# Performance work log

Measured on AMD Instinct MI355X. Metric: run time of the kernel, lower is better.

## Reference

```python
import jax, jax.numpy as jnp
import numpy as np

T, S, B, H, NH, F = 256, 128, 32, 1024, 16, 4096
D = H // NH  # head dim


def setup_inputs() -> dict:
    key = jax.random.key(0)
    ks = jax.random.split(key, 14)
    w = lambda k, shape: jax.random.normal(k, shape, jnp.float32) * 0.02
    return {
        "x": jax.random.normal(ks[0], (T, B, H), jnp.float32),
        "src_bias": jnp.zeros((B, 1, 1, S), jnp.float32),
        "tgt_bias": jnp.zeros((B, 1, 1, T), jnp.float32),
        "memory": jax.random.normal(ks[1], (S, B, H), jnp.float32),
        # cross-attention projections
        "Wq": w(ks[2], (H, H)), "bq": jnp.zeros((H,), jnp.float32),
        "Wk": w(ks[3], (H, H)), "bk": jnp.zeros((H,), jnp.float32),
        "Wv": w(ks[4], (H, H)), "bv": jnp.zeros((H,), jnp.float32),
        "Wo": w(ks[5], (H, H)), "bo": jnp.zeros((H,), jnp.float32),
        # feed-forward
        "W1": w(ks[6], (H, F)), "b1": jnp.zeros((F,), jnp.float32),
        "W2": w(ks[7], (F, H)), "b2": jnp.zeros((H,), jnp.float32),
        # LSTM gates: input = cat(ffn_x, attn_ctx, h) -> 3H, output 4H (i,j,f,o)
        "Wg": w(ks[8], (3 * H, 4 * H)), "bg": jnp.zeros((4 * H,), jnp.float32),
    }


def _cross_attention(xq, mem, bias, Wq, bq, Wk, bk, Wv, bv, Wo, bo):
    # xq: [B,T,H], mem: [B,S,H], bias: [B,1,1,S]
    b, t, h = xq.shape
    q = (xq @ Wq + bq).reshape(b, t, NH, D) * (D ** -0.5)
    k = (mem @ Wk + bk).reshape(b, -1, NH, D)
    v = (mem @ Wv + bv).reshape(b, -1, NH, D)
    logits = jnp.einsum("bqhd,bkhd->bhqk", q, k) + bias
    wts = jax.nn.softmax(logits, axis=-1)
    ctx = jnp.einsum("bhqk,bkhd->bqhd", wts, v).reshape(b, t, h)
    return ctx @ Wo + bo


def reference(x, src_bias, tgt_bias, memory, Wq, bq, Wk, bk, Wv, bv, Wo, bo,
              W1, b1, W2, b2, Wg, bg):
    # cross attention (time-major -> batch-major -> time-major)
    c_attn = _cross_attention(jnp.transpose(x, (1, 0, 2)),
                              jnp.transpose(memory, (1, 0, 2)),
                              src_bias, Wq, bq, Wk, bk, Wv, bv, Wo, bo)
    c_attn = jnp.transpose(c_attn, (1, 0, 2))  # [T,B,H]

    # feed-forward on x (dropout disabled / eval mode)
    ffn_x = jax.nn.relu(x @ W1 + b1) @ W2 + b2  # [T,B,H]

    xs = jnp.concatenate([ffn_x, c_attn], axis=-1)  # [T,B,2H]
    c0 = jnp.zeros((x.shape[1], H), x.dtype)
    h0 = jnp.zeros((x.shape[1], H), x.dtype)

    def step(carry, xt):
        c, h = carry
        g = jnp.concatenate([xt, h], axis=-1) @ Wg + bg  # [B,4H]
        i = jax.nn.sigmoid(g[:, :H])
        j = jnp.tanh(g[:, H:2 * H])
        f = jax.nn.sigmoid(g[:, 2 * H:3 * H])
        o = jax.nn.sigmoid(g[:, 3 * H:])
        new_c = f * c + i * j
        new_h = o * new_c  # THUMT LSTMCell default activation=None
        return (new_c, new_h), new_h

    (c_f, h_f), hiddens = jax.lax.scan(step, (c0, h0), xs)
    return hiddens, c_f, h_f
```

## Files before the change

### kernel.cpp

```cpp
#include <hip/hip_runtime.h>
#include <cstdint>
#include <cstddef>

#define T_  256
#define S_  128
#define B_  32
#define H_  1024
#define NH_ 16
#define D_  64
#define F_  4096
#define TB_ (T_*B_)
#define SB_ (S_*B_)

typedef unsigned short u16;
typedef unsigned int   u32;
typedef unsigned long long u64;
typedef __attribute__((ext_vector_type(8))) short s16x8;
typedef __attribute__((ext_vector_type(4))) float f32x4;
typedef __attribute__((ext_vector_type(4))) u32  u32x4;

static __device__ __forceinline__ float b2f(u16 u) {
  union { u32 i; float f; } cv; cv.i = ((u32)u) << 16; return cv.f;
}
static __device__ __forceinline__ u16 f2b(float f) {
  union { float f; u32 i; } cv; cv.f = f;
  u32 u = cv.i;
  u32 r = (u + 0x7fffu + ((u >> 16) & 1u)) >> 16;
  return (u16)r;
}
static __device__ __forceinline__ float sigm(float x) {
  return 1.0f / (1.0f + __expf(-x));
}
static __device__ __forceinline__ float tanh_fast(float x) {
  float e2 = __expf(2.0f * x);
  return 1.0f - 2.0f / (e2 + 1.0f);
}

typedef const __attribute__((address_space(1))) void* gvoidp;
typedef __attribute__((address_space(3))) void* lvoidp;
static __device__ __forceinline__ void gl_lds16(const void* g, void* l) {
  __builtin_amdgcn_global_load_lds((gvoidp)g, (lvoidp)l, 16, 0, 0);
}

static __device__ __forceinline__ void cast_task(const float* __restrict__ in,
                                                 u16* __restrict__ out, int lb, int tid) {
  int i = lb * 256 + tid;
  float4 v = reinterpret_cast<const float4*>(in)[i];
  ushort4 o;
  o.x = f2b(v.x); o.y = f2b(v.y); o.z = f2b(v.z); o.w = f2b(v.w);
  reinterpret_cast<ushort4*>(out)[i] = o;
}

static __device__ __forceinline__ void tr32(const float* __restrict__ in,
                                            u16* __restrict__ out,
                                            int R, int C, int lin, int tid,
                                            float tile[32][33]) {
  const int gx = C >> 5;
  const int bx = lin % gx, by = lin / gx;
  const int c0 = bx << 5, r0 = by << 5;
  const int tx = tid & 31, ty = tid >> 5;
  #pragma unroll
  for (int k = 0; k < 32; k += 8)
    tile[ty + k][tx] = in[(size_t)(r0 + ty + k) * C + c0 + tx];
  __syncthreads();
  #pragma unroll
  for (int k = 0; k < 32; k += 8)
    out[(size_t)(c0 + ty + k) * R + r0 + tx] = f2b(tile[tx][ty + k]);
}

#define NB_SENT 1
#define NB_CX   8192
#define NB_CM   4096
#define NB_TSQ  1024
#define NB_TW1  4096
#define NB_TW2  4096
#define NB_TGX  8192
#define NB_TWH  4096
#define NB_PREP (NB_SENT + NB_CX + NB_CM + 4*NB_TSQ + NB_TW1 + NB_TW2 + NB_TGX + NB_TWH)

__global__ __launch_bounds__(256) void prep_all(
    const float* __restrict__ x, const float* __restrict__ mem,
    const float* __restrict__ Wq, const float* __restrict__ Wk,
    const float* __restrict__ Wv, const float* __restrict__ Wo,
    const float* __restrict__ W1, const float* __restrict__ W2,
    const float* __restrict__ Wg,
    u16* __restrict__ xb, u16* __restrict__ memb,
    u16* __restrict__ WqT, u16* __restrict__ WkT, u16* __restrict__ WvT,
    u16* __restrict__ WoT, u16* __restrict__ W1T, u16* __restrict__ W2T,
    u16* __restrict__ WgxT, u16* __restrict__ WhT, u32* __restrict__ sent)
{
  __shared__ float tile[32][33];
  int b = blockIdx.x;
  const int tid = threadIdx.x;
  if (b < NB_SENT) { sent[tid] = 0; sent[tid + 256] = 0; return; }
  b -= NB_SENT;
  if (b < NB_CX) { cast_task(x, xb, b, tid); return; }      b -= NB_CX;
  if (b < NB_CM) { cast_task(mem, memb, b, tid); return; }  b -= NB_CM;
  if (b < NB_TSQ) { tr32(Wq, WqT, H_, H_, b, tid, tile); return; }  b -= NB_TSQ;
  if (b < NB_TSQ) { tr32(Wk, WkT, H_, H_, b, tid, tile); return; }  b -= NB_TSQ;
  if (b < NB_TSQ) { tr32(Wv, WvT, H_, H_, b, tid, tile); return; }  b -= NB_TSQ;
  if (b < NB_TSQ) { tr32(Wo, WoT, H_, H_, b, tid, tile); return; }  b -= NB_TSQ;
  if (b < NB_TW1) { tr32(W1, W1T, H_, F_, b, tid, tile); return; }  b -= NB_TW1;
  if (b < NB_TW2) { tr32(W2, W2T, F_, H_, b, tid, tile); return; }  b -= NB_TW2;
  if (b < NB_TGX) { tr32(Wg, WgxT, 2 * H_, 4 * H_, b, tid, tile); return; } b -= NB_TGX;
  tr32(Wg + (size_t)(2 * H_) * (4 * H_), WhT, H_, 4 * H_, b, tid, tile);
}

#define SBAR      asm volatile("s_barrier" ::: "memory")
#define VMCNT4    asm volatile("s_waitcnt vmcnt(4)" ::: "memory")
#define VMCNT0    asm volatile("s_waitcnt vmcnt(0)" ::: "memory")

struct GJob {
  const u16* A; const u16* Bt; u16* Out; const float* bias;
  int Kdim; int ostride; int relu; int gridx; int nblk; float scale;
};
struct GBatch { GJob j[4]; int starts[4]; int njobs; };

static __device__ __forceinline__ void stage_region(
    const u16* __restrict__ src, int Kdim, int row0,
    int kt, int kh, char* lds_region, int tid) {
  const int w  = tid >> 6;
  const int r  = tid >> 2;
  const int cs = (tid & 3) ^ ((tid >> 3) & 3);
  const int kbase = kt * 64 + kh * 32 + cs * 8;
  gl_lds16(src + (size_t)(row0 + r) * Kdim + kbase,        lds_region + w * 1024);
  gl_lds16(src + (size_t)(row0 + 128 + r) * Kdim + kbase,  lds_region + 8192 + w * 1024);
}

static __device__ __forceinline__ s16x8 ldsf(const char* sm, int base, int row, int quad) {
  return *(const s16x8*)(sm + base + row * 64 + ((quad ^ ((row >> 1) & 3)) << 4));
}

__global__ __launch_bounds__(512, 2) void gemm256(GBatch gb)
{
  __shared__ __align__(16) u16 smem[65536];
  char* sm = (char*)smem;
  const int bid = blockIdx.x;
  int ji = 0;
  #pragma unroll
  for (int t = 1; t < 4; t++)
    if (t < gb.njobs && bid >= gb.starts[t]) ji = t;
  const GJob J = gb.j[ji];
  const int lin = bid - gb.starts[ji];
  const int wg = (lin & 7) * (J.nblk >> 3) + (lin >> 3);
  const int bx = wg % J.gridx, by = wg / J.gridx;
  const int bm = by << 8, bn = bx << 8;

  const int tid = threadIdx.x;
  const int wavei = tid >> 6, lane = tid & 63;
  const int quad = lane >> 4, l16 = lane & 15;
  const int wm = wavei >> 2, wn = wavei & 3;
  const int NT = J.Kdim >> 6;
  const int arow = wm * 128;
  const int brow = wn * 64;

  f32x4 acc[8][4] = {};

  stage_region(J.A,  J.Kdim, bm, 0, 0, sm + 0,     tid);
  stage_region(J.Bt, J.Kdim, bn, 0, 0, sm + 32768, tid);
  stage_region(J.A,  J.Kdim, bm, 0, 1, sm + 16384, tid);
  stage_region(J.Bt, J.Kdim, bn, 0, 1, sm + 49152, tid);
  VMCNT4;
  SBAR;

  for (int kt = 0; kt < NT; kt++) {
    const int p = (kt & 1) << 16;
    const int q = p ^ 65536;
    const int Ab = p, Bb = p + 32768;
    const bool st = (kt + 1 < NT);
    s16x8 af[8], b0, b1;

    #pragma unroll
    for (int mi = 0; mi < 8; mi++)
      af[mi] = ldsf(sm, Ab, arow + mi * 16 + l16, quad);
    b0 = ldsf(sm, Bb, brow + l16, quad);
    b1 = ldsf(sm, Bb, brow + 16 + l16, quad);
    if (st) stage_region(J.A, J.Kdim, bm, kt + 1, 0, sm + q, tid);
    SBAR;
    __builtin_amdgcn_s_setprio(1);
    #pragma unroll
    for (int mi = 0; mi < 8; mi++) {
      acc[mi][0] = __builtin_amdgcn_mfma_f32_16x16x32_bf16(af[mi], b0, acc[mi][0], 0, 0, 0);
      acc[mi][1] = __builtin_amdgcn_mfma_f32_16x16x32_bf16(af[mi], b1, acc[mi][1], 0, 0, 0);
    }
    __builtin_amdgcn_s_setprio(0);
    SBAR;

    b0 = ldsf(sm, Bb, brow + 32 + l16, quad);
    b1 = ldsf(sm, Bb, brow + 48 + l16, quad);
    if (st) stage_region(J.Bt, J.Kdim, bn, kt + 1, 0, sm + q + 32768, tid);
    SBAR;
    __builtin_amdgcn_s_setprio(1);
    #pragma unroll
    for (int mi = 0; mi < 8; mi++) {
      acc[mi][2] = __builtin_amdgcn_mfma_f32_16x16x32_bf16(af[mi], b0, acc[mi][2], 0, 0, 0);
      acc[mi][3] = __builtin_amdgcn_mfma_f32_16x16x32_bf16(af[mi], b1, acc[mi][3], 0, 0, 0);
    }
    __builtin_amdgcn_s_setprio(0);
    if (st) { VMCNT4; } else { VMCNT0; }
    SBAR;

    const int Ab1 = Ab + 16384, Bb1 = Bb + 16384;
    #pragma unroll
    for (int mi = 0; mi < 8; mi++)
      af[mi] = ldsf(sm, Ab1, arow + mi * 16 + l16, quad);
    b0 = ldsf(sm, Bb1, brow + l16, quad);
    b1 = ldsf(sm, Bb1, brow + 16 + l16, quad);
    if (st) stage_region(J.A, J.Kdim, bm, kt + 1, 1, sm + q + 16384, tid);
    SBAR;
    __builtin_amdgcn_s_setprio(1);
    #pragma unroll
    for (int mi = 0; mi < 8; mi++) {
      acc[mi][0] = __builtin_amdgcn_mfma_f32_16x16x32_bf16(af[mi], b0, acc[mi][0], 0, 0, 0);
      acc[mi][1] = __builtin_amdgcn_mfma_f32_16x16x32_bf16(af[mi], b1, acc[mi][1], 0, 0, 0);
    }
    __builtin_amdgcn_s_setprio(0);
    SBAR;

    b0 = ldsf(sm, Bb1, brow + 32 + l16, quad);
    b1 = ldsf(sm, Bb1, brow + 48 + l16, quad);
    if (st) stage_region(J.Bt, J.Kdim, bn, kt + 1, 1, sm + q + 49152, tid);
    SBAR;
    __builtin_amdgcn_s_setprio(1);
    #pragma unroll
    for (int mi = 0; mi < 8; mi++) {
      acc[mi][2] = __builtin_amdgcn_mfma_f32_16x16x32_bf16(af[mi], b0, acc[mi][2], 0, 0, 0);
      acc[mi][3] = __builtin_amdgcn_mfma_f32_16x16x32_bf16(af[mi], b1, acc[mi][3], 0, 0, 0);
    }
    __builtin_amdgcn_s_setprio(0);
    if (st) { VMCNT4; }
    SBAR;
  }

  #pragma unroll
  for (int mi = 0; mi < 8; mi++) {
    #pragma unroll
    for (int nj = 0; nj < 4; nj++) {
      const int colo = bn + wn * 64 + nj * 16 + l16;
      const float bv = J.bias[colo];
      #pragma unroll
      for (int r = 0; r < 4; r++) {
        const int rowo = bm + wm * 128 + mi * 16 + quad * 4 + r;
        float vv = (acc[mi][nj][r] + bv) * J.scale;
        if (J.relu) vv = fmaxf(vv, 0.0f);
        J.Out[(size_t)rowo * J.ostride + colo] = f2b(vv);
      }
    }
  }
}

__global__ __launch_bounds__(256) void attn_kernel(
    const u16* __restrict__ q, const u16* __restrict__ k, const u16* __restrict__ v,
    const float* __restrict__ src_bias, u16* __restrict__ ctx)
{
  __shared__ u16 ks[S_ * D_];
  __shared__ u16 vs[S_ * D_];
  const int b  = blockIdx.x >> 4;
  const int nh = blockIdx.x & 15;
  const int tid = threadIdx.x;

  for (int i = tid; i < (S_ * D_) / 8; i += 256) {
    int s = i >> 3, c = (i & 7) * 8;
    *(uint4*)&ks[s * D_ + c] = *(const uint4*)&k[((size_t)(s * B_ + b)) * H_ + nh * D_ + c];
    *(uint4*)&vs[s * D_ + c] = *(const uint4*)&v[((size_t)(s * B_ + b)) * H_ + nh * D_ + c];
  }
  __syncthreads();

  const int t = tid;
  float qf[D_];
  const u16* qp = &q[((size_t)(t * B_ + b)) * H_ + nh * D_];
  #pragma unroll
  for (int c8 = 0; c8 < D_; c8 += 8) {
    uint4 qv = *(const uint4*)&qp[c8];
    const u16* pu = (const u16*)&qv;
    #pragma unroll
    for (int j = 0; j < 8; j++) qf[c8 + j] = b2f(pu[j]);
  }
  const float* bias = src_bias + b * S_;

  float m = -1e30f, l = 0.0f;
  for (int s = 0; s < S_; s++) {
    float dot = 0.0f;
    #pragma unroll
    for (int d = 0; d < D_; d++) dot += qf[d] * b2f(ks[s * D_ + d]);
    dot += bias[s];
    float nm = fmaxf(m, dot);
    l = l * __expf(m - nm) + __expf(dot - nm);
    m = nm;
  }
  float of[D_] = {};
  const float inv = 1.0f / l;
  for (int s = 0; s < S_; s++) {
    float dot = 0.0f;
    #pragma unroll
    for (int d = 0; d < D_; d++) dot += qf[d] * b2f(ks[s * D_ + d]);
    dot += bias[s];
    float w = __expf(dot - m) * inv;
    #pragma unroll
    for (int d = 0; d < D_; d++) of[d] += w * b2f(vs[s * D_ + d]);
  }
  u16* op = &ctx[((size_t)(t * B_ + b)) * H_ + nh * D_];
  #pragma unroll
  for (int c8 = 0; c8 < D_; c8 += 8) {
    u16 tmp[8];
    #pragma unroll
    for (int j = 0; j < 8; j++) tmp[j] = f2b(of[c8 + j]);
    *(uint4*)&op[c8] = *(const uint4*)tmp;
  }
}

#define ISSUE2(K) { \
  const u16* b0_ = hb + ((size_t)(wave * 16 + (K) * 2 + (quad >> 1))) * 512 + \
                   (quad & 1) * 8 + l16 * 16; \
  asm volatile("global_load_dwordx4 %0, %1, off sc0 sc1" : "=v"(ba[K][0]) : "v"(b0_) : "memory"); \
  asm volatile("global_load_dwordx4 %0, %1, off sc0 sc1" : "=v"(ba[K][1]) : "v"(b0_ + 256) : "memory"); }

#define DO_MFMA(A0,A1,KC)                                                           \
  { _Pragma("unroll") for (int g_ = 0; g_ < 3; g_++) {                              \
      s16x8 wf_ = *(const s16x8*)&Wl[wave][((g_ * 8 + (KC)) * 64 + lane) * 8];      \
      acc[g_][0] = __builtin_amdgcn_mfma_f32_16x16x32_bf16(A0, wf_, acc[g_][0], 0, 0, 0); \
      acc[g_][1] = __builtin_amdgcn_mfma_f32_16x16x32_bf16(A1, wf_, acc[g_][1], 0, 0, 0); } \
    acc[3][0] = __builtin_amdgcn_mfma_f32_16x16x32_bf16(A0, wo[KC], acc[3][0], 0, 0, 0);  \
    acc[3][1] = __builtin_amdgcn_mfma_f32_16x16x32_bf16(A1, wo[KC], acc[3][1], 0, 0, 0); }

#define CONSUME(K, NSTR) { \
  asm volatile("s_waitcnt vmcnt(" NSTR ")" ::: "memory"); \
  __builtin_amdgcn_sched_barrier(0); \
  DO_MFMA(ba[K][0], ba[K][1], K); }

__global__ __launch_bounds__(256, 1) void lstm_persistent(
    const u16* __restrict__ g_x, const u16* __restrict__ WhT,
    u16* __restrict__ hb16, u32* __restrict__ sent, float* __restrict__ out)
{
  __shared__ __align__(16) u16 Wl[4][3 * 8 * 64 * 8];
  __shared__ float P[4][4][32][17];
  const int bk = blockIdx.x, tid = threadIdx.x;
  const int wave = tid >> 6, lane = tid & 63;
  const int quad = lane >> 4, l16 = lane & 15;

  for (int i = lane; i < 3 * 8 * 64; i += 64) {
    const int g  = (i >> 9) & 3;
    const int kc = (i >> 6) & 7;
    const int row = g * H_ + bk * 16 + (lane & 15);
    const int col = wave * 256 + kc * 32 + (lane >> 4) * 8;
    *(uint4*)&Wl[wave][i * 8] = *(const uint4*)&WhT[(size_t)row * H_ + col];
  }
  s16x8 wo[8];
  {
    const int row = 3 * H_ + bk * 16 + (lane & 15);
    const int colb = wave * 256 + (lane >> 4) * 8;
    #pragma unroll
    for (int kc = 0; kc < 8; kc++)
      wo[kc] = *(const s16x8*)&WhT[(size_t)row * H_ + colb + kc * 32];
  }
  __syncthreads();

  const int pb = tid >> 4, pc = tid & 15;
  const int col = bk * 16 + pc;
  float creg[2] = {0.0f, 0.0f};

  float gxp[2][4];
  #pragma unroll
  for (int ii = 0; ii < 2; ii++)
    #pragma unroll
    for (int g = 0; g < 4; g++)
      gxp[ii][g] = b2f(g_x[((size_t)(pb + ii * 16)) * (4 * H_) + g * H_ + col]);

  s16x8 ba[8][2];

  for (int t = 0; t < T_; t++) {
    if (t > 0) {
      const u32 st = (u32)t;
      const u16* hb = hb16 + ((t & 1) ^ 1) * 32768;

      { const u32* sp = sent + ((size_t)(((t & 1) ^ 1) * 256 + wave * 64 + lane));
        u32 sv;
        do {
          asm volatile("global_load_dword %0, %1, off sc0 sc1\n\ts_waitcnt vmcnt(0)"
                       : "=v"(sv) : "v"(sp) : "memory");
        } while (!__all(sv == st)); }

      f32x4 acc[4][2] = {};
      ISSUE2(0) ISSUE2(1) ISSUE2(2) ISSUE2(3)
      ISSUE2(4) ISSUE2(5) ISSUE2(6) ISSUE2(7)
      CONSUME(0, "14") CONSUME(1, "12") CONSUME(2, "10") CONSUME(3, "8")
      CONSUME(4, "6")  CONSUME(5, "4")  CONSUME(6, "2")  CONSUME(7, "0")

      #pragma unroll
      for (int g = 0; g < 4; g++)
        #pragma unroll
        for (int mt = 0; mt < 2; mt++)
          #pragma unroll
          for (int r = 0; r < 4; r++)
            P[wave][g][mt * 16 + quad * 4 + r][l16] = acc[g][mt][r];
    }
    __syncthreads();

    float gs[2][4];
    #pragma unroll
    for (int ii = 0; ii < 2; ii++) {
      const int b_ = pb + ii * 16;
      #pragma unroll
      for (int g = 0; g < 4; g++) {
        float s = gxp[ii][g];
        if (t > 0) s += P[0][g][b_][pc] + P[1][g][b_][pc] + P[2][g][b_][pc] + P[3][g][b_][pc];
        gs[ii][g] = s;
      }
    }
    __syncthreads();

    float hn[2], cn[2];
    #pragma unroll
    for (int ii = 0; ii < 2; ii++) {
      const float iv = sigm(gs[ii][0]);
      const float jv = tanh_fast(gs[ii][1]);
      const float fv = sigm(gs[ii][2]);
      const float ov = sigm(gs[ii][3]);
      cn[ii] = fv * creg[ii] + iv * jv;
      hn[ii] = ov * cn[ii];
      creg[ii] = cn[ii];
    }

    {
      u32 lo0 = f2b(hn[0]), lo1 = f2b(hn[1]);
      u32 hi0 = __shfl_down(lo0, 1), hi1 = __shfl_down(lo1, 1);
      if ((pc & 1) == 0) {
        u32* hw32 = (u32*)(hb16 + (t & 1) * 32768);
        u32 dw0 = lo0 | (hi0 << 16);
        u32 dw1 = lo1 | (hi1 << 16);
        __hip_atomic_store(&hw32[(size_t)bk * 256 + pb * 8 + (pc >> 1)], dw0,
                           __ATOMIC_RELAXED, __HIP_MEMORY_SCOPE_AGENT);
        __hip_atomic_store(&hw32[(size_t)bk * 256 + (pb + 16) * 8 + (pc >> 1)], dw1,
                           __ATOMIC_RELAXED, __HIP_MEMORY_SCOPE_AGENT);
      }
      asm volatile("s_waitcnt vmcnt(0)" ::: "memory");
      if (lane == 0)
        __hip_atomic_store(&sent[(size_t)(t & 1) * 256 + bk * 4 + wave], (u32)(t + 1),
                           __ATOMIC_RELAXED, __HIP_MEMORY_SCOPE_AGENT);
    }

    #pragma unroll
    for (int ii = 0; ii < 2; ii++) {
      const int b_ = pb + ii * 16;
      out[(size_t)t * (B_ * H_) + b_ * H_ + col] = hn[ii];
      if (t == T_ - 1) {
        out[(size_t)T_ * B_ * H_ + b_ * H_ + col] = cn[ii];
        out[(size_t)T_ * B_ * H_ + B_ * H_ + b_ * H_ + col] = hn[ii];
      }
    }
    if (t < T_ - 1) {
      #pragma unroll
      for (int ii = 0; ii < 2; ii++)
        #pragma unroll
        for (int g = 0; g < 4; g++)
          gxp[ii][g] = b2f(g_x[((size_t)(t + 1) * B_ + pb + ii * 16) * (4 * H_) + g * H_ + col]);
    }
  }
}

extern "C" void kernel_launch(void* const* d_in, const int* in_sizes, int n_in,
                              void* d_out, int out_size, void* d_ws, size_t ws_size,
                              hipStream_t stream)
{
  const float* x        = (const float*)d_in[0];
  const float* src_bias = (const float*)d_in[1];
  const float* mem      = (const float*)d_in[3];
  const float* Wq = (const float*)d_in[4];  const float* bq = (const float*)d_in[5];
  const float* Wk = (const float*)d_in[6];  const float* bk = (const float*)d_in[7];
  const float* Wv = (const float*)d_in[8];  const float* bv = (const float*)d_in[9];
  const float* Wo = (const float*)d_in[10]; const float* bo = (const float*)d_in[11];
  const float* W1 = (const float*)d_in[12]; const float* b1f = (const float*)d_in[13];
  const float* W2 = (const float*)d_in[14]; const float* b2f_ = (const float*)d_in[15];
  const float* Wg = (const float*)d_in[16]; const float* bg = (const float*)d_in[17];
  float* out = (float*)d_out;

  char* p = (char*)d_ws;
  u16* xb   = (u16*)p; p += (size_t)TB_ * H_ * 2;
  u16* memb = (u16*)p; p += (size_t)SB_ * H_ * 2;
  u16* WqT  = (u16*)p; p += (size_t)H_ * H_ * 2;
  u16* WkT  = (u16*)p; p += (size_t)H_ * H_ * 2;
  u16* WvT  = (u16*)p; p += (size_t)H_ * H_ * 2;
  u16* WoT  = (u16*)p; p += (size_t)H_ * H_ * 2;
  u16* W1T  = (u16*)p; p += (size_t)F_ * H_ * 2;
  u16* W2T  = (u16*)p; p += (size_t)H_ * F_ * 2;
  u16* WgxT = (u16*)p; p += (size_t)(4 * H_) * (2 * H_) * 2;
  u16* WhT  = (u16*)p; p += (size_t)(4 * H_) * H_ * 2;
  u16* qb   = (u16*)p; p += (size_t)TB_ * H_ * 2;
  u16* kb   = (u16*)p; p += (size_t)SB_ * H_ * 2;
  u16* vb   = (u16*)p; p += (size_t)SB_ * H_ * 2;
  u16* ctxb = (u16*)p; p += (size_t)TB_ * H_ * 2;
  u16* xs   = (u16*)p; p += (size_t)TB_ * (2 * H_) * 2;
  u16* h1   = (u16*)p; p += (size_t)TB_ * F_ * 2;
  u16* hb16 = (u16*)p; p += (size_t)2 * 32768 * 2;
  u32* sent = (u32*)p; p += (size_t)2 * 256 * 4;
  u16* gx   = h1;

  prep_all<<<dim3(NB_PREP), dim3(256), 0, stream>>>(
      x, mem, Wq, Wk, Wv, Wo, W1, W2, Wg,
      xb, memb, WqT, WkT, WvT, WoT, W1T, W2T, WgxT, WhT, sent);

  GBatch gb1 = {};
  gb1.j[0] = { xb,   WqT, qb, bq,  H_, H_, 0, H_ / 256, (TB_ / 256) * (H_ / 256), 0.125f };
  gb1.j[1] = { memb, WkT, kb, bk,  H_, H_, 0, H_ / 256, (SB_ / 256) * (H_ / 256), 1.0f   };
  gb1.j[2] = { memb, WvT, vb, bv,  H_, H_, 0, H_ / 256, (SB_ / 256) * (H_ / 256), 1.0f   };
  gb1.j[3] = { xb,   W1T, h1, b1f, H_, F_, 1, F_ / 256, (TB_ / 256) * (F_ / 256), 1.0f   };
  gb1.starts[0] = 0;
  gb1.starts[1] = gb1.j[0].nblk;
  gb1.starts[2] = gb1.starts[1] + gb1.j[1].nblk;
  gb1.starts[3] = gb1.starts[2] + gb1.j[2].nblk;
  gb1.njobs = 4;
  const int nb1 = gb1.starts[3] + gb1.j[3].nblk;
  gemm256<<<dim3(nb1), dim3(512), 0, stream>>>(gb1);

  attn_kernel<<<dim3(B_ * NH_), dim3(256), 0, stream>>>(qb, kb, vb, src_bias, ctxb);

  GBatch gb2 = {};
  gb2.j[0] = { ctxb, WoT, xs + H_, bo,   H_, 2 * H_, 0, H_ / 256, (TB_ / 256) * (H_ / 256), 1.0f };
  gb2.j[1] = { h1,   W2T, xs,      b2f_, F_, 2 * H_, 0, H_ / 256, (TB_ / 256) * (H_ / 256), 1.0f };
  gb2.starts[0] = 0;
  gb2.starts[1] = gb2.j[0].nblk;
  gb2.njobs = 2;
  const int nb2 = gb2.starts[1] + gb2.j[1].nblk;
  gemm256<<<dim3(nb2), dim3(512), 0, stream>>>(gb2);

  GBatch gb3 = {};
  gb3.j[0] = { xs, WgxT, gx, bg, 2 * H_, 4 * H_, 0, 4 * H_ / 256, (TB_ / 256) * (4 * H_ / 256), 1.0f };
  gb3.starts[0] = 0;
  gb3.njobs = 1;
  gemm256<<<dim3(gb3.j[0].nblk), dim3(512), 0, stream>>>(gb3);

  lstm_persistent<<<dim3(64), dim3(256), 0, stream>>>(gx, WhT, hb16, sent, out);
}
```

Measured before the change: 1.591 ms.

## Fuse gate-input GEMM into persistent LSTM kernel with per-tile readiness flags

Merges the final gate-input GEMM and the persistent LSTM recurrence into one launch. 64 blocks run the recurrence while the other 512 blocks compute the gx tiles in row order and publish per-tile ready flags. The recurrence polls a flag every 8 timesteps before loading gx, so it can start before the whole GEMM is done and the two overlap. In exchange the LSTM blocks now use 512 threads with half idle, LDS grows, and correctness depends on the LSTM blocks being co-resident with the GEMM blocks.

```diff
diff --git a/kernel.cpp b/kernel.cpp
--- a/kernel.cpp
+++ b/kernel.cpp
@@ -87,12 +87,17 @@
     u16* __restrict__ xb, u16* __restrict__ memb,
     u16* __restrict__ WqT, u16* __restrict__ WkT, u16* __restrict__ WvT,
     u16* __restrict__ WoT, u16* __restrict__ W1T, u16* __restrict__ W2T,
-    u16* __restrict__ WgxT, u16* __restrict__ WhT, u32* __restrict__ sent)
+    u16* __restrict__ WgxT, u16* __restrict__ WhT, u32* __restrict__ sent,
+    u32* __restrict__ gxs)
 {
   __shared__ float tile[32][33];
   int b = blockIdx.x;
   const int tid = threadIdx.x;
-  if (b < NB_SENT) { sent[tid] = 0; sent[tid + 256] = 0; return; }
+  if (b < NB_SENT) {
+    sent[tid] = 0; sent[tid + 256] = 0;
+    gxs[tid] = 0;  gxs[tid + 256] = 0;
+    return;
+  }
   b -= NB_SENT;
   if (b < NB_CX) { cast_task(x, xb, b, tid); return; }      b -= NB_CX;
   if (b < NB_CM) { cast_task(mem, memb, b, tid); return; }  b -= NB_CM;
@@ -129,6 +134,93 @@
 
 static __device__ __forceinline__ s16x8 ldsf(const char* sm, int base, int row, int quad) {
   return *(const s16x8*)(sm + base + row * 64 + ((quad ^ ((row >> 1) & 3)) << 4));
+}
+
+static __device__ __forceinline__ void gemm_compute(
+    const GJob& J, int bm, int bn, char* sm, f32x4 (&acc)[8][4], int tid)
+{
+  const int wavei = tid >> 6, lane = tid & 63;
+  const int quad = lane >> 4, l16 = lane & 15;
+  const int wm = wavei >> 2, wn = wavei & 3;
+  const int NT = J.Kdim >> 6;
+  const int arow = wm * 128;
+  const int brow = wn * 64;
+
+  stage_region(J.A,  J.Kdim, bm, 0, 0, sm + 0,     tid);
+  stage_region(J.Bt, J.Kdim, bn, 0, 0, sm + 32768, tid);
+  stage_region(J.A,  J.Kdim, bm, 0, 1, sm + 16384, tid);
+  stage_region(J.Bt, J.Kdim, bn, 0, 1, sm + 49152, tid);
+  VMCNT4;
+  SBAR;
+
+  for (int kt = 0; kt < NT; kt++) {
+    const int p = (kt & 1) << 16;
+    const int q = p ^ 65536;
+    const int Ab = p, Bb = p + 32768;
+    const bool st = (kt + 1 < NT);
+    s16x8 af[8], b0, b1;
+
+    #pragma unroll
+    for (int mi = 0; mi < 8; mi++)
+      af[mi] = ldsf(sm, Ab, arow + mi * 16 + l16, quad);
+    b0 = ldsf(sm, Bb, brow + l16, quad);
+    b1 = ldsf(sm, Bb, brow + 16 + l16, quad);
+    if (st) stage_region(J.A, J.Kdim, bm, kt + 1, 0, sm + q, tid);
+    SBAR;
+    __builtin_amdgcn_s_setprio(1);
+    #pragma unroll
+    for (int mi = 0; mi < 8; mi++) {
+      acc[mi][0] = __builtin_amdgcn_mfma_f32_16x16x32_bf16(af[mi], b0, acc[mi][0], 0, 0, 0);
+      acc[mi][1] = __builtin_amdgcn_mfma_f32_16x16x32_bf16(af[mi], b1, acc[mi][1], 0, 0, 0);
+    }
+    __builtin_amdgcn_s_setprio(0);
+    SBAR;
+
+    b0 = ldsf(sm, Bb, brow + 32 + l16, quad);
+    b1 = ldsf(sm, Bb, brow + 48 + l16, quad);
+    if (st) stage_region(J.Bt, J.Kdim, bn, kt + 1, 0, sm + q + 32768, tid);
+    SBAR;
+    __builtin_amdgcn_s_setprio(1);
+    #pragma unroll
+    for (int mi = 0; mi < 8; mi++) {
+      acc[mi][2] = __builtin_amdgcn_mfma_f32_16x16x32_bf16(af[mi], b0, acc[mi][2], 0, 0, 0);
+      acc[mi][3] = __builtin_amdgcn_mfma_f32_16x16x32_bf16(af[mi], b1, acc[mi][3], 0, 0, 0);
+    }
+    __builtin_amdgcn_s_setprio(0);
+    if (st) { VMCNT4; } else { VMCNT0; }
+    SBAR;
+
+    const int Ab1 = Ab + 16384, Bb1 = Bb + 16384;
+    #pragma unroll
+    for (int mi = 0; mi < 8; mi++)
+      af[mi] = ldsf(sm, Ab1, arow + mi * 16 + l16, quad);
+    b0 = ldsf(sm, Bb1, brow + l16, quad);
+    b1 = ldsf(sm, Bb1, brow + 16 + l16, quad);
+    if (st) stage_region(J.A, J.Kdim, bm, kt + 1, 1, sm + q + 16384, tid);
+    SBAR;
+    __builtin_amdgcn_s_setprio(1);
+    #pragma unroll
+    for (int mi = 0; mi < 8; mi++) {
+      acc[mi][0] = __builtin_amdgcn_mfma_f32_16x16x32_bf16(af[mi], b0, acc[mi][0], 0, 0, 0);
+      acc[mi][1] = __builtin_amdgcn_mfma_f32_16x16x32_bf16(af[mi], b1, acc[mi][1], 0, 0, 0);
+    }
+    __builtin_amdgcn_s_setprio(0);
+    SBAR;
+
+    b0 = ldsf(sm, Bb1, brow + 32 + l16, quad);
+    b1 = ldsf(sm, Bb1, brow + 48 + l16, quad);
+    if (st) stage_region(J.Bt, J.Kdim, bn, kt + 1, 1, sm + q + 49152, tid);
+    SBAR;
+    __builtin_amdgcn_s_setprio(1);
+    #pragma unroll
+    for (int mi = 0; mi < 8; mi++) {
+      acc[mi][2] = __builtin_amdgcn_mfma_f32_16x16x32_bf16(af[mi], b0, acc[mi][2], 0, 0, 0);
+      acc[mi][3] = __builtin_amdgcn_mfma_f32_16x16x32_bf16(af[mi], b1, acc[mi][3], 0, 0, 0);
+    }
+    __builtin_amdgcn_s_setprio(0);
+    if (st) { VMCNT4; }
+    SBAR;
+  }
 }
 
 __global__ __launch_bounds__(512, 2) void gemm256(GBatch gb)
@@ -145,92 +237,13 @@
   const int wg = (lin & 7) * (J.nblk >> 3) + (lin >> 3);
   const int bx = wg % J.gridx, by = wg / J.gridx;
   const int bm = by << 8, bn = bx << 8;
-
   const int tid = threadIdx.x;
   const int wavei = tid >> 6, lane = tid & 63;
   const int quad = lane >> 4, l16 = lane & 15;
   const int wm = wavei >> 2, wn = wavei & 3;
-  const int NT = J.Kdim >> 6;
-  const int arow = wm * 128;
-  const int brow = wn * 64;
 
   f32x4 acc[8][4] = {};
-
-  stage_region(J.A,  J.Kdim, bm, 0, 0, sm + 0,     tid);
-  stage_region(J.Bt, J.Kdim, bn, 0, 0, sm + 32768, tid);
-  stage_region(J.A,  J.Kdim, bm, 0, 1, sm + 16384, tid);
-  stage_region(J.Bt, J.Kdim, bn, 0, 1, sm + 49152, tid);
-  VMCNT4;
-  SBAR;
-
-  for (int kt = 0; kt < NT; kt++) {
-    const int p = (kt & 1) << 16;
-    const int q = p ^ 65536;
-    const int Ab = p, Bb = p + 32768;
-    const bool st = (kt + 1 < NT);
-    s16x8 af[8], b0, b1;
-
-    #pragma unroll
-    for (int mi = 0; mi < 8; mi++)
-      af[mi] = ldsf(sm, Ab, arow + mi * 16 + l16, quad);
-    b0 = ldsf(sm, Bb, brow + l16, quad);
-    b1 = ldsf(sm, Bb, brow + 16 + l16, quad);
-    if (st) stage_region(J.A, J.Kdim, bm, kt + 1, 0, sm + q, tid);
-    SBAR;
-    __builtin_amdgcn_s_setprio(1);
-    #pragma unroll
-    for (int mi = 0; mi < 8; mi++) {
-      acc[mi][0] = __builtin_amdgcn_mfma_f32_16x16x32_bf16(af[mi], b0, acc[mi][0], 0, 0, 0);
-      acc[mi][1] = __builtin_amdgcn_mfma_f32_16x16x32_bf16(af[mi], b1, acc[mi][1], 0, 0, 0);
-    }
-    __builtin_amdgcn_s_setprio(0);
-    SBAR;
-
-    b0 = ldsf(sm, Bb, brow + 32 + l16, quad);
-    b1 = ldsf(sm, Bb, brow + 48 + l16, quad);
-    if (st) stage_region(J.Bt, J.Kdim, bn, kt + 1, 0, sm + q + 32768, tid);
-    SBAR;
-    __builtin_amdgcn_s_setprio(1);
-    #pragma unroll
-    for (int mi = 0; mi < 8; mi++) {
-      acc[mi][2] = __builtin_amdgcn_mfma_f32_16x16x32_bf16(af[mi], b0, acc[mi][2], 0, 0, 0);
-      acc[mi][3] = __builtin_amdgcn_mfma_f32_16x16x32_bf16(af[mi], b1, acc[mi][3], 0, 0, 0);
-    }
-    __builtin_amdgcn_s_setprio(0);
-    if (st) { VMCNT4; } else { VMCNT0; }
-    SBAR;
-
-    const int Ab1 = Ab + 16384, Bb1 = Bb + 16384;
-    #pragma unroll
-    for (int mi = 0; mi < 8; mi++)
-      af[mi] = ldsf(sm, Ab1, arow + mi * 16 + l16, quad);
-    b0 = ldsf(sm, Bb1, brow + l16, quad);
-    b1 = ldsf(sm, Bb1, brow + 16 + l16, quad);
-    if (st) stage_region(J.A, J.Kdim, bm, kt + 1, 1, sm + q + 16384, tid);
-    SBAR;
-    __builtin_amdgcn_s_setprio(1);
-    #pragma unroll
-    for (int mi = 0; mi < 8; mi++) {
-      acc[mi][0] = __builtin_amdgcn_mfma_f32_16x16x32_bf16(af[mi], b0, acc[mi][0], 0, 0, 0);
-      acc[mi][1] = __builtin_amdgcn_mfma_f32_16x16x32_bf16(af[mi], b1, acc[mi][1], 0, 0, 0);
-    }
-    __builtin_amdgcn_s_setprio(0);
-    SBAR;
-
-    b0 = ldsf(sm, Bb1, brow + 32 + l16, quad);
-    b1 = ldsf(sm, Bb1, brow + 48 + l16, quad);
-    if (st) stage_region(J.Bt, J.Kdim, bn, kt + 1, 1, sm + q + 49152, tid);
-    SBAR;
-    __builtin_amdgcn_s_setprio(1);
-    #pragma unroll
-    for (int mi = 0; mi < 8; mi++) {
-      acc[mi][2] = __builtin_amdgcn_mfma_f32_16x16x32_bf16(af[mi], b0, acc[mi][2], 0, 0, 0);
-      acc[mi][3] = __builtin_amdgcn_mfma_f32_16x16x32_bf16(af[mi], b1, acc[mi][3], 0, 0, 0);
-    }
-    __builtin_amdgcn_s_setprio(0);
-    if (st) { VMCNT4; }
-    SBAR;
-  }
+  gemm_compute(J, bm, bn, sm, acc, tid);
 
   #pragma unroll
   for (int mi = 0; mi < 8; mi++) {
@@ -309,6 +322,8 @@
   }
 }
 
+#define WAIT0A asm volatile("s_waitcnt vmcnt(0)" ::: "memory")
+
 #define ISSUE2(K) { \
   const u16* b0_ = hb + ((size_t)(wave * 16 + (K) * 2 + (quad >> 1))) * 512 + \
                    (quad & 1) * 8 + l16 * 16; \
@@ -317,36 +332,91 @@
 
 #define DO_MFMA(A0,A1,KC)                                                           \
   { _Pragma("unroll") for (int g_ = 0; g_ < 3; g_++) {                              \
-      s16x8 wf_ = *(const s16x8*)&Wl[wave][((g_ * 8 + (KC)) * 64 + lane) * 8];      \
-      acc[g_][0] = __builtin_amdgcn_mfma_f32_16x16x32_bf16(A0, wf_, acc[g_][0], 0, 0, 0); \
-      acc[g_][1] = __builtin_amdgcn_mfma_f32_16x16x32_bf16(A1, wf_, acc[g_][1], 0, 0, 0); } \
-    acc[3][0] = __builtin_amdgcn_mfma_f32_16x16x32_bf16(A0, wo[KC], acc[3][0], 0, 0, 0);  \
-    acc[3][1] = __builtin_amdgcn_mfma_f32_16x16x32_bf16(A1, wo[KC], acc[3][1], 0, 0, 0); }
+      s16x8 wf_ = *(const s16x8*)&Wl[wave * 12288 + ((g_ * 8 + (KC)) * 64 + lane) * 8]; \
+      acc2[g_][0] = __builtin_amdgcn_mfma_f32_16x16x32_bf16(A0, wf_, acc2[g_][0], 0, 0, 0); \
+      acc2[g_][1] = __builtin_amdgcn_mfma_f32_16x16x32_bf16(A1, wf_, acc2[g_][1], 0, 0, 0); } \
+    acc2[3][0] = __builtin_amdgcn_mfma_f32_16x16x32_bf16(A0, wo[KC], acc2[3][0], 0, 0, 0);  \
+    acc2[3][1] = __builtin_amdgcn_mfma_f32_16x16x32_bf16(A1, wo[KC], acc2[3][1], 0, 0, 0); }
 
 #define CONSUME(K, NSTR) { \
   asm volatile("s_waitcnt vmcnt(" NSTR ")" ::: "memory"); \
   __builtin_amdgcn_sched_barrier(0); \
   DO_MFMA(ba[K][0], ba[K][1], K); }
 
-__global__ __launch_bounds__(256, 1) void lstm_persistent(
-    const u16* __restrict__ g_x, const u16* __restrict__ WhT,
-    u16* __restrict__ hb16, u32* __restrict__ sent, float* __restrict__ out)
+#define PIDX(W,G,ROW,C) ((((W) * 4 + (G)) * 32 + (ROW)) * 17 + (C))
+
+#define ISSUE_GX(TT) { \
+  _Pragma("unroll") for (int ii_ = 0; ii_ < 2; ii_++) \
+    _Pragma("unroll") for (int g_ = 0; g_ < 4; g_++) { \
+      const u16* gp_ = g_x + ((size_t)((TT) * B_ + pb + ii_ * 16)) * (4 * H_) + g_ * H_ + col; \
+      asm volatile("global_load_ushort %0, %1, off sc0 sc1" : "=v"(gq[ii_ * 4 + g_]) : "v"(gp_) : "memory"); } }
+
+#define CVT_GX() { \
+  _Pragma("unroll") for (int ii_ = 0; ii_ < 2; ii_++) \
+    _Pragma("unroll") for (int g_ = 0; g_ < 4; g_++) \
+      gxp[ii_][g_] = b2f((u16)gq[ii_ * 4 + g_]); }
+
+#define POLLGXS(RB) { \
+  const u32* sp_ = gxs + (RB) * 16 + (lane & 3) * 4 + (bk >> 4); \
+  u32 sv_; \
+  do { asm volatile("global_load_dword %0, %1, off sc0 sc1\n\ts_waitcnt vmcnt(0)" \
+                    : "=v"(sv_) : "v"(sp_) : "memory"); } while (!__all(sv_ != 0)); }
+
+__global__ __launch_bounds__(512, 1) void gate_lstm(
+    GBatch gb, const u16* __restrict__ g_x, const u16* __restrict__ WhT,
+    u16* __restrict__ hb16, u32* __restrict__ sent, u32* __restrict__ gxs,
+    float* __restrict__ out)
 {
-  __shared__ __align__(16) u16 Wl[4][3 * 8 * 64 * 8];
-  __shared__ float P[4][4][32][17];
-  const int bk = blockIdx.x, tid = threadIdx.x;
+  __shared__ __align__(16) char smem[133120];
+  const int tid = threadIdx.x;
+
+  if (blockIdx.x >= 64) {
+    const GJob J = gb.j[0];
+    const int lin = blockIdx.x - 64;
+    const int bx = lin & 15, by = lin >> 4;
+    const int bm = by << 8, bn = bx << 8;
+    const int wavei = tid >> 6, lane = tid & 63;
+    const int quad = lane >> 4, l16 = lane & 15;
+    const int wm = wavei >> 2, wn = wavei & 3;
+    f32x4 acc[8][4] = {};
+    gemm_compute(J, bm, bn, smem, acc, tid);
+    #pragma unroll
+    for (int mi = 0; mi < 8; mi++) {
+      #pragma unroll
+      for (int nj = 0; nj < 4; nj++) {
+        const int colo = bn + wn * 64 + nj * 16 + l16;
+        const float bv = J.bias[colo];
+        #pragma unroll
+        for (int r = 0; r < 4; r++) {
+          const int rowo = bm + wm * 128 + mi * 16 + quad * 4 + r;
+          u32 hv = f2b(acc[mi][nj][r] + bv);
+          u16* op_ = J.Out + (size_t)rowo * J.ostride + colo;
+          asm volatile("global_store_short %0, %1, off sc0 sc1" :: "v"(op_), "v"(hv) : "memory");
+        }
+      }
+    }
+    WAIT0A;
+    __syncthreads();
+    if (tid == 0)
+      __hip_atomic_store(&gxs[by * 16 + bx], 1u, __ATOMIC_RELAXED, __HIP_MEMORY_SCOPE_AGENT);
+    return;
+  }
+
+  const int bk = blockIdx.x;
   const int wave = tid >> 6, lane = tid & 63;
   const int quad = lane >> 4, l16 = lane & 15;
-
-  for (int i = lane; i < 3 * 8 * 64; i += 64) {
-    const int g  = (i >> 9) & 3;
-    const int kc = (i >> 6) & 7;
-    const int row = g * H_ + bk * 16 + (lane & 15);
-    const int col = wave * 256 + kc * 32 + (lane >> 4) * 8;
-    *(uint4*)&Wl[wave][i * 8] = *(const uint4*)&WhT[(size_t)row * H_ + col];
-  }
+  u16*   Wl = (u16*)smem;
+  float* P  = (float*)(smem + 98304);
+
   s16x8 wo[8];
-  {
+  if (tid < 256) {
+    for (int i = lane; i < 3 * 8 * 64; i += 64) {
+      const int g  = (i >> 9) & 3;
+      const int kc = (i >> 6) & 7;
+      const int row = g * H_ + bk * 16 + (lane & 15);
+      const int cw  = wave * 256 + kc * 32 + (lane >> 4) * 8;
+      *(uint4*)&Wl[wave * 12288 + i * 8] = *(const uint4*)&WhT[(size_t)row * H_ + cw];
+    }
     const int row = 3 * H_ + bk * 16 + (lane & 15);
     const int colb = wave * 256 + (lane >> 4) * 8;
     #pragma unroll
@@ -358,29 +428,32 @@
   const int pb = tid >> 4, pc = tid & 15;
   const int col = bk * 16 + pc;
   float creg[2] = {0.0f, 0.0f};
-
   float gxp[2][4];
-  #pragma unroll
-  for (int ii = 0; ii < 2; ii++)
-    #pragma unroll
-    for (int g = 0; g < 4; g++)
-      gxp[ii][g] = b2f(g_x[((size_t)(pb + ii * 16)) * (4 * H_) + g * H_ + col]);
-
+  u32 gq[8];
   s16x8 ba[8][2];
 
+  if (tid < 256) {
+    POLLGXS(0);
+    ISSUE_GX(0);
+    WAIT0A;
+    __builtin_amdgcn_sched_barrier(0);
+    CVT_GX();
+  }
+
   for (int t = 0; t < T_; t++) {
-    if (t > 0) {
+    if (tid < 256 && t > 0) {
       const u32 st = (u32)t;
       const u16* hb = hb16 + ((t & 1) ^ 1) * 32768;
-
       { const u32* sp = sent + ((size_t)(((t & 1) ^ 1) * 256 + wave * 64 + lane));
         u32 sv;
         do {
           asm volatile("global_load_dword %0, %1, off sc0 sc1\n\ts_waitcnt vmcnt(0)"
                        : "=v"(sv) : "v"(sp) : "memory");
         } while (!__all(sv == st)); }
-
-      f32x4 acc[4][2] = {};
+      __builtin_amdgcn_sched_barrier(0);
+      CVT_GX();
+
+      f32x4 acc2[4][2] = {};
       ISSUE2(0) ISSUE2(1) ISSUE2(2) ISSUE2(3)
       ISSUE2(4) ISSUE2(5) ISSUE2(6) ISSUE2(7)
       CONSUME(0, "14") CONSUME(1, "12") CONSUME(2, "10") CONSUME(3, "8")
@@ -392,68 +465,70 @@
         for (int mt = 0; mt < 2; mt++)
           #pragma unroll
           for (int r = 0; r < 4; r++)
-            P[wave][g][mt * 16 + quad * 4 + r][l16] = acc[g][mt][r];
+            P[PIDX(wave, g, mt * 16 + quad * 4 + r, l16)] = acc2[g][mt][r];
     }
     __syncthreads();
 
     float gs[2][4];
-    #pragma unroll
-    for (int ii = 0; ii < 2; ii++) {
-      const int b_ = pb + ii * 16;
+    if (tid < 256) {
       #pragma unroll
-      for (int g = 0; g < 4; g++) {
-        float s = gxp[ii][g];
-        if (t > 0) s += P[0][g][b_][pc] + P[1][g][b_][pc] + P[2][g][b_][pc] + P[3][g][b_][pc];
-        gs[ii][g] = s;
+      for (int ii = 0; ii < 2; ii++) {
+        const int b_ = pb + ii * 16;
+        #pragma unroll
+        for (int g = 0; g < 4; g++) {
+          float s = gxp[ii][g];
+          if (t > 0) s += P[PIDX(0, g, b_, pc)] + P[PIDX(1, g, b_, pc)]
+                        + P[PIDX(2, g, b_, pc)] + P[PIDX(3, g, b_, pc)];
+          gs[ii][g] = s;
+        }
       }
     }
     __syncthreads();
 
-    float hn[2], cn[2];
-    #pragma unroll
-    for (int ii = 0; ii < 2; ii++) {
-      const float iv = sigm(gs[ii][0]);
-      const float jv = tanh_fast(gs[ii][1]);
-      const float fv = sigm(gs[ii][2]);
-      const float ov = sigm(gs[ii][3]);
-      cn[ii] = fv * creg[ii] + iv * jv;
-      hn[ii] = ov * cn[ii];
-      creg[ii] = cn[ii];
-    }
-
-    {
-      u32 lo0 = f2b(hn[0]), lo1 = f2b(hn[1]);
-      u32 hi0 = __shfl_down(lo0, 1), hi1 = __shfl_down(lo1, 1);
-      if ((pc & 1) == 0) {
-        u32* hw32 = (u32*)(hb16 + (t & 1) * 32768);
-        u32 dw0 = lo0 | (hi0 << 16);
-        u32 dw1 = lo1 | (hi1 << 16);
-        __hip_atomic_store(&hw32[(size_t)bk * 256 + pb * 8 + (pc >> 1)], dw0,
-                           __ATOMIC_RELAXED, __HIP_MEMORY_SCOPE_AGENT);
-        __hip_atomic_store(&hw32[(size_t)bk * 256 + (pb + 16) * 8 + (pc >> 1)], dw1,
-                           __ATOMIC_RELAXED, __HIP_MEMORY_SCOPE_AGENT);
+    if (tid < 256) {
+      float hn[2], cn[2];
+      #pragma unroll
+      for (int ii = 0; ii < 2; ii++) {
+        const float iv = sigm(gs[ii][0]);
+        const float jv = tanh_fast(gs[ii][1]);
+        const float fv = sigm(gs[ii][2]);
+        const float ov = sigm(gs[ii][3]);
+        cn[ii] = fv * creg[ii] + iv * jv;
+        hn[ii] = ov * cn[ii];
+        creg[ii] = cn[ii];
       }
-      asm volatile("s_waitcnt vmcnt(0)" ::: "memory");
-      if (lane == 0)
-        __hip_atomic_store(&sent[(size_t)(t & 1) * 256 + bk * 4 + wave], (u32)(t + 1),
-                           __ATOMIC_RELAXED, __HIP_MEMORY_SCOPE_AGENT);
-    }
-
-    #pragma unroll
-    for (int ii = 0; ii < 2; ii++) {
-      const int b_ = pb + ii * 16;
-      out[(size_t)t * (B_ * H_) + b_ * H_ + col] = hn[ii];
-      if (t == T_ - 1) {
-        out[(size_t)T_ * B_ * H_ + b_ * H_ + col] = cn[ii];
-        out[(size_t)T_ * B_ * H_ + B_ * H_ + b_ * H_ + col] = hn[ii];
+
+      {
+        u32 lo0 = f2b(hn[0]), lo1 = f2b(hn[1]);
+        u32 hi0 = __shfl_down(lo0, 1), hi1 = __shfl_down(lo1, 1);
+        if ((pc & 1) == 0) {
+          u32* hw32 = (u32*)(hb16 + (t & 1) * 32768);
+          u32 dw0 = lo0 | (hi0 << 16);
+          u32 dw1 = lo1 | (hi1 << 16);
+          __hip_atomic_store(&hw32[(size_t)bk * 256 + pb * 8 + (pc >> 1)], dw0,
+                             __ATOMIC_RELAXED, __HIP_MEMORY_SCOPE_AGENT);
+          __hip_atomic_store(&hw32[(size_t)bk * 256 + (pb + 16) * 8 + (pc >> 1)], dw1,
+                             __ATOMIC_RELAXED, __HIP_MEMORY_SCOPE_AGENT);
+        }
+        WAIT0A;
+        if (lane == 0)
+          __hip_atomic_store(&sent[(size_t)(t & 1) * 256 + bk * 4 + wave], (u32)(t + 1),
+                             __ATOMIC_RELAXED, __HIP_MEMORY_SCOPE_AGENT);
       }
-    }
-    if (t < T_ - 1) {
+
       #pragma unroll
-      for (int ii = 0; ii < 2; ii++)
-        #pragma unroll
-        for (int g = 0; g < 4; g++)
-          gxp[ii][g] = b2f(g_x[((size_t)(t + 1) * B_ + pb + ii * 16) * (4 * H_) + g * H_ + col]);
+      for (int ii = 0; ii < 2; ii++) {
+        const int b_ = pb + ii * 16;
+        out[(size_t)t * (B_ * H_) + b_ * H_ + col] = hn[ii];
+        if (t == T_ - 1) {
+          out[(size_t)T_ * B_ * H_ + b_ * H_ + col] = cn[ii];
+          out[(size_t)T_ * B_ * H_ + B_ * H_ + b_ * H_ + col] = hn[ii];
+        }
+      }
+      if (t < T_ - 1) {
+        if (((t + 1) & 7) == 0) POLLGXS((t + 1) >> 3);
+        ISSUE_GX(t + 1);
+      }
     }
   }
 }
@@ -493,11 +568,12 @@
   u16* h1   = (u16*)p; p += (size_t)TB_ * F_ * 2;
   u16* hb16 = (u16*)p; p += (size_t)2 * 32768 * 2;
   u32* sent = (u32*)p; p += (size_t)2 * 256 * 4;
+  u32* gxs  = (u32*)p; p += (size_t)512 * 4;
   u16* gx   = h1;
 
   prep_all<<<dim3(NB_PREP), dim3(256), 0, stream>>>(
       x, mem, Wq, Wk, Wv, Wo, W1, W2, Wg,
-      xb, memb, WqT, WkT, WvT, WoT, W1T, W2T, WgxT, WhT, sent);
+      xb, memb, WqT, WkT, WvT, WoT, W1T, W2T, WgxT, WhT, sent, gxs);
 
   GBatch gb1 = {};
   gb1.j[0] = { xb,   WqT, qb, bq,  H_, H_, 0, H_ / 256, (TB_ / 256) * (H_ / 256), 0.125f };
@@ -524,10 +600,9 @@
   gemm256<<<dim3(nb2), dim3(512), 0, stream>>>(gb2);
 
   GBatch gb3 = {};
-  gb3.j[0] = { xs, WgxT, gx, bg, 2 * H_, 4 * H_, 0, 4 * H_ / 256, (TB_ / 256) * (4 * H_ / 256), 1.0f };
+  gb3.j[0] = { xs, WgxT, gx, bg, 2 * H_, 4 * H_, 0, 16, 512, 1.0f };
   gb3.starts[0] = 0;
   gb3.njobs = 1;
-  gemm256<<<dim3(gb3.j[0].nblk), dim3(512), 0, stream>>>(gb3);
-
-  lstm_persistent<<<dim3(64), dim3(256), 0, stream>>>(gx, WhT, hb16, sent, out);
-}
+  gate_lstm<<<dim3(64 + 512), dim3(512), 0, stream>>>(
+      gb3, gx, WhT, hb16, sent, gxs, out);
+}
```

Result: slower. 1.715 ms (+7.8%).
